# Optimization experiments

Measured on AMD Instinct MI355X. Metric: run time of the kernel, lower is better.

Reference implementation:

```python
import jax, jax.numpy as jnp
import numpy as np

N_EMB = 64
N_HEAD = 8
HEAD = N_EMB // N_HEAD
BLOCK = 64
EPS = 1e-5


def setup_inputs() -> dict:
    key = jax.random.key(0)
    ks = jax.random.split(key, 12)
    B, T, C = 4096, 64, N_EMB
    s = 0.02
    return {
        "x": jax.random.normal(ks[0], (B, T, C), jnp.float32),
        "ln1_w": jnp.ones((C,), jnp.float32),
        "ln1_b": jnp.zeros((C,), jnp.float32),
        # stacked per-head projections, layout [H, C_in, head_size] (x @ W)
        "wq": jax.random.normal(ks[1], (N_HEAD, C, HEAD), jnp.float32) * s,
        "wk": jax.random.normal(ks[2], (N_HEAD, C, HEAD), jnp.float32) * s,
        "wv": jax.random.normal(ks[3], (N_HEAD, C, HEAD), jnp.float32) * s,
        "proj_w": jax.random.normal(ks[4], (C, C), jnp.float32) * s,
        "proj_b": jnp.zeros((C,), jnp.float32),
        "ln2_w": jnp.ones((C,), jnp.float32),
        "ln2_b": jnp.zeros((C,), jnp.float32),
        "fc1_w": jax.random.normal(ks[5], (C, 4 * C), jnp.float32) * s,
        "fc1_b": jnp.zeros((4 * C,), jnp.float32),
        "fc2_w": jax.random.normal(ks[6], (4 * C, C), jnp.float32) * s,
        "fc2_b": jnp.zeros((C,), jnp.float32),
    }


def _layernorm(x, w, b):
    mu = jnp.mean(x, axis=-1, keepdims=True)
    var = jnp.mean((x - mu) ** 2, axis=-1, keepdims=True)
    return (x - mu) * jax.lax.rsqrt(var + EPS) * w + b


def reference(x, ln1_w, ln1_b, wq, wk, wv, proj_w, proj_b,
              ln2_w, ln2_b, fc1_w, fc1_b, fc2_w, fc2_b):
    B, T, C = x.shape
    # --- self-attention branch (dropout in eval mode => identity) ---
    h = _layernorm(x, ln1_w, ln1_b)
    q = jnp.einsum("btc,hcd->bhtd", h, wq)
    k = jnp.einsum("btc,hcd->bhtd", h, wk)
    v = jnp.einsum("btc,hcd->bhtd", h, wv)
    # NOTE: original scales by C**-0.5 (full embed dim), not head_size**-0.5
    scores = jnp.einsum("bhtd,bhsd->bhts", q, k) * (C ** -0.5)
    causal = jnp.tril(jnp.ones((T, T), bool))
    scores = jnp.where(causal, scores, -jnp.inf)
    w = jax.nn.softmax(scores, axis=-1)
    attn = jnp.einsum("bhts,bhsd->bhtd", w, v)  # [B,H,T,hs]
    attn = attn.transpose(0, 2, 1, 3).reshape(B, T, C)  # concat heads
    x = x + attn @ proj_w + proj_b
    # --- feed-forward branch ---
    h2 = _layernorm(x, ln2_w, ln2_b)
    ff = jax.nn.relu(h2 @ fc1_w + fc1_b) @ fc2_w + fc2_b
    return x + ff
```

## Files before the change

kernel.cpp:

```cpp
#include <hip/hip_runtime.h>

typedef __attribute__((ext_vector_type(8))) short bf16x8;
typedef __attribute__((ext_vector_type(4))) float f32x4;
typedef __attribute__((ext_vector_type(2))) unsigned int u32x2;
typedef __attribute__((ext_vector_type(4))) unsigned int u32x4;

__device__ __forceinline__ unsigned short f2bf(float f) {
  return __builtin_bit_cast(unsigned short, (__bf16)f);
}
__device__ __forceinline__ unsigned pk2(float a, float b) {
  return (unsigned)f2bf(a) | ((unsigned)f2bf(b) << 16);
}
__device__ __forceinline__ float bf2f(unsigned short h) {
  unsigned u = ((unsigned)h) << 16;
  return __builtin_bit_cast(float, u);
}
__device__ __forceinline__ bf16x8 frag(u32x4 v) { return __builtin_bit_cast(bf16x8, v); }

#if __has_builtin(__builtin_amdgcn_exp2f)
#define EXP2(x) __builtin_amdgcn_exp2f(x)
#else
#define EXP2(x) exp2f(x)
#endif

__device__ __forceinline__ void wfence() {
  asm volatile("" ::: "memory");
  __builtin_amdgcn_wave_barrier();
}

#define MFMA16(a, b, c) __builtin_amdgcn_mfma_f32_16x16x32_bf16(a, b, c, 0, 0, 0)

#define LR 72
#define OFF_VT 4608
#define OFF_Q  9216
#define ZROW   13824
#define OFF_WST 13904
#define LDS_TOT (13904 + 12288)

#define WS_H2 65536
#define WS_X2 (65536 + 16777216)

__global__ void prep_weights(const float* __restrict__ wq, const float* __restrict__ wk,
                             const float* __restrict__ wv, const float* __restrict__ projw,
                             const float* __restrict__ fc1w, const float* __restrict__ fc2w,
                             unsigned short* __restrict__ ws) {
  int c = blockIdx.x, l = threadIdx.x;
  int g = l >> 4, jl = l & 15;
  int kind, T, ks;
  if (c < 8)       { kind = 0; T = c >> 1;        ks = c & 1; }
  else if (c < 16) { kind = 1; T = (c - 8) >> 1;  ks = (c - 8) & 1; }
  else if (c < 24) { kind = 2; T = (c - 16) >> 1; ks = (c - 16) & 1; }
  else if (c < 32) { kind = 3; T = (c - 24) >> 1; ks = (c - 24) & 1; }
  else if (c < 64) { kind = 4; T = (c - 32) >> 1; ks = (c - 32) & 1; }
  else             { kind = 5; T = (c - 64) >> 3; ks = (c - 64) & 7; }
  int n = 16 * T + jl;
  unsigned short* dst = ws + c * 512 + l * 8;
  #pragma unroll
  for (int jj = 0; jj < 8; ++jj) {
    int kp = 16 * (2 * (ks & 1) + (jj >> 2)) + 4 * g + (jj & 3);
    int kn = 32 * ks + 8 * g + jj;
    float v;
    if (kind == 0)      v = wq[(n >> 3) * 512 + kp * 8 + (n & 7)] * 0.18033688011f;
    else if (kind == 1) v = wk[(n >> 3) * 512 + kp * 8 + (n & 7)];
    else if (kind == 2) v = wv[(n >> 3) * 512 + kp * 8 + (n & 7)];
    else if (kind == 3) v = projw[kn * 64 + n];
    else if (kind == 4) v = fc1w[kp * 256 + n];
    else                v = fc2w[(64 * (ks >> 1) + kp) * 64 + n];
    dst[jj] = f2bf(v);
  }
}

__global__ __launch_bounds__(256, 3) void block_attn(
    const float* __restrict__ x,
    const float* __restrict__ ln1w, const float* __restrict__ ln1b,
    const float* __restrict__ projb,
    const float* __restrict__ ln2w, const float* __restrict__ ln2b,
    unsigned short* __restrict__ wsm) {
  __shared__ __attribute__((aligned(16))) unsigned short lds[LDS_TOT];

  const int tid  = threadIdx.x;
  const int w    = tid >> 6;
  const int lane = tid & 63;
  const int g    = lane >> 4;
  const int jl   = lane & 15;
  const size_t b = blockIdx.x;
  const float* xb = x + b * 4096;
  const f32x4 zf = {0.f, 0.f, 0.f, 0.f};

  const int myrow = 16 * w + jl;
  const int krow  = myrow * LR;
  const int qrow  = OFF_Q + myrow * LR;
  const int sigb  = 32 * (w >> 1) + 8 * g + 4 * (w & 1);

  const u32x4* wsrc = (const u32x4*)wsm;
  u32x4 stg0 = wsrc[0 * 256 + tid], stg1 = wsrc[1 * 256 + tid];
  u32x4 stg2 = wsrc[2 * 256 + tid], stg3 = wsrc[3 * 256 + tid];
  u32x4 stg4 = wsrc[4 * 256 + tid], stg5 = wsrc[5 * 256 + tid];

  f32x4 xw[4];
  float mean, rstd;
  unsigned hr[8];
  {
    float s = 0.f, ss = 0.f;
    #pragma unroll
    for (int mi = 0; mi < 4; ++mi) {
      xw[mi] = *(const f32x4*)(xb + myrow * 64 + 16 * mi + 4 * g);
      #pragma unroll
      for (int r = 0; r < 4; ++r) { s += xw[mi][r]; ss += xw[mi][r] * xw[mi][r]; }
    }
    s  += __shfl_xor(s, 16, 64);  s  += __shfl_xor(s, 32, 64);
    ss += __shfl_xor(ss, 16, 64); ss += __shfl_xor(ss, 32, 64);
    mean = s * 0.015625f;
    rstd = rsqrtf(ss * 0.015625f - mean * mean + 1e-5f);
    #pragma unroll
    for (int mi = 0; mi < 4; ++mi) {
      f32x4 lw = *(const f32x4*)(ln1w + 16 * mi + 4 * g);
      f32x4 lb = *(const f32x4*)(ln1b + 16 * mi + 4 * g);
      float o0 = (xw[mi][0] - mean) * rstd * lw[0] + lb[0];
      float o1 = (xw[mi][1] - mean) * rstd * lw[1] + lb[1];
      float o2 = (xw[mi][2] - mean) * rstd * lw[2] + lb[2];
      float o3 = (xw[mi][3] - mean) * rstd * lw[3] + lb[3];
      hr[2 * mi] = pk2(o0, o1); hr[2 * mi + 1] = pk2(o2, o3);
    }
  }
  bf16x8 hb0 = frag((u32x4){hr[0], hr[1], hr[2], hr[3]});
  bf16x8 hb1 = frag((u32x4){hr[4], hr[5], hr[6], hr[7]});

  {
    u32x4* wdst = (u32x4*)(lds + OFF_WST);
    wdst[0 * 256 + tid] = stg0; wdst[1 * 256 + tid] = stg1;
    wdst[2 * 256 + tid] = stg2; wdst[3 * 256 + tid] = stg3;
    wdst[4 * 256 + tid] = stg4; wdst[5 * 256 + tid] = stg5;
  }
  if (tid < 40) ((unsigned*)(lds + ZROW))[tid] = 0u;
  __syncthreads();

  #pragma clang loop unroll(disable)
  for (int mt = 0; mt < 4; ++mt) {
    const unsigned short* wq8 = lds + OFF_WST + (2 * mt) * 512 + lane * 8;
    bf16x8 aq0 = *(const bf16x8*)(wq8);
    bf16x8 aq1 = *(const bf16x8*)(wq8 + 512);
    bf16x8 ak0 = *(const bf16x8*)(wq8 + 8 * 512);
    bf16x8 ak1 = *(const bf16x8*)(wq8 + 9 * 512);
    bf16x8 bv0 = *(const bf16x8*)(wq8 + 16 * 512);
    bf16x8 bv1 = *(const bf16x8*)(wq8 + 17 * 512);
    f32x4 q = MFMA16(aq0, hb0, zf); q = MFMA16(aq1, hb1, q);
    *(u32x2*)(lds + qrow + 16 * mt + 4 * g) = (u32x2){pk2(q[0], q[1]), pk2(q[2], q[3])};
    f32x4 kk = MFMA16(ak0, hb0, zf); kk = MFMA16(ak1, hb1, kk);
    *(u32x2*)(lds + krow + 16 * mt + 4 * g) = (u32x2){pk2(kk[0], kk[1]), pk2(kk[2], kk[3])};
    f32x4 vv = MFMA16(hb0, bv0, zf); vv = MFMA16(hb1, bv1, vv);
    *(u32x2*)(lds + OFF_VT + (16 * mt + jl) * LR + sigb) =
        (u32x2){pk2(vv[0], vv[1]), pk2(vv[2], vv[3])};
  }
  __syncthreads();

  {
    const bool g0 = (g == 0), j8 = (jl < 8);
    const int ka0 = g0 ? ((0  + jl) * LR) : ZROW;
    const int ka1 = g0 ? ((16 + jl) * LR) : ZROW;
    const int ka2 = g0 ? ((32 + jl) * LR) : ZROW;
    const int ka3 = g0 ? ((48 + jl) * LR) : ZROW;
    const int qb0 = g0 ? (OFF_Q + (0  + jl) * LR) : ZROW;
    const int qb1 = g0 ? (OFF_Q + (16 + jl) * LR) : ZROW;
    const int qb2 = g0 ? (OFF_Q + (32 + jl) * LR) : ZROW;
    const int qb3 = g0 ? (OFF_Q + (48 + jl) * LR) : ZROW;
    const bool m0 = (4 * g + 0 <= jl), m1 = (4 * g + 1 <= jl);
    const bool m2 = (4 * g + 2 <= jl), m3 = (4 * g + 3 <= jl);
    #pragma clang loop unroll(disable)
    for (int hh = 0; hh < 2; ++hh) {
      const int ho = 16 * w + 8 * hh;
      const int vbase = j8 ? (OFF_VT + (ho + jl) * LR) : ZROW;
      bf16x8 bq0 = *(const bf16x8*)(lds + qb0 + ho);
      bf16x8 bq1 = *(const bf16x8*)(lds + qb1 + ho);
      bf16x8 bq2 = *(const bf16x8*)(lds + qb2 + ho);
      bf16x8 bq3 = *(const bf16x8*)(lds + qb3 + ho);
      bf16x8 k0  = *(const bf16x8*)(lds + ka0 + ho);
      bf16x8 k1  = *(const bf16x8*)(lds + ka1 + ho);
      bf16x8 k2  = *(const bf16x8*)(lds + ka2 + ho);
      bf16x8 k3  = *(const bf16x8*)(lds + ka3 + ho);
      bf16x8 aw0 = *(const bf16x8*)(lds + vbase + 8 * g);
      bf16x8 aw1 = *(const bf16x8*)(lds + vbase + 32 + 8 * g);
      wfence();
      f32x4 s00 = MFMA16(k0, bq0, zf);
      f32x4 s10 = MFMA16(k0, bq1, zf);
      f32x4 s11 = MFMA16(k1, bq1, zf);
      {
        float e0 = m0 ? EXP2(s00[0]) : 0.f, e1 = m1 ? EXP2(s00[1]) : 0.f;
        float e2 = m2 ? EXP2(s00[2]) : 0.f, e3 = m3 ? EXP2(s00[3]) : 0.f;
        float sum = (e0 + e1) + (e2 + e3);
        sum += __shfl_xor(sum, 16, 64); sum += __shfl_xor(sum, 32, 64);
        float inv = __builtin_amdgcn_rcpf(sum);
        bf16x8 bp0 = frag((u32x4){pk2(e0, e1), pk2(e2, e3), 0u, 0u});
        f32x4 pv = MFMA16(aw0, bp0, zf);
        if (g < 2)
          *(u32x2*)(lds + OFF_Q + jl * LR + ho + 4 * g) =
              (u32x2){pk2(pv[0] * inv, pv[1] * inv), pk2(pv[2] * inv, pv[3] * inv)};
      }
      {
        float a0 = EXP2(s10[0]), a1 = EXP2(s10[1]);
        float a2 = EXP2(s10[2]), a3 = EXP2(s10[3]);
        float e0 = m0 ? EXP2(s11[0]) : 0.f, e1 = m1 ? EXP2(s11[1]) : 0.f;
        float e2 = m2 ? EXP2(s11[2]) : 0.f, e3 = m3 ? EXP2(s11[3]) : 0.f;
        float sum = ((a0 + a1) + (a2 + a3)) + ((e0 + e1) + (e2 + e3));
        sum += __shfl_xor(sum, 16, 64); sum += __shfl_xor(sum, 32, 64);
        float inv = __builtin_amdgcn_rcpf(sum);
        bf16x8 bp0 = frag((u32x4){pk2(a0, a1), pk2(a2, a3), pk2(e0, e1), pk2(e2, e3)});
        f32x4 pv = MFMA16(aw0, bp0, zf);
        if (g < 2)
          *(u32x2*)(lds + OFF_Q + (16 + jl) * LR + ho + 4 * g) =
              (u32x2){pk2(pv[0] * inv, pv[1] * inv), pk2(pv[2] * inv, pv[3] * inv)};
      }
      f32x4 s20 = MFMA16(k0, bq2, zf);
      f32x4 s21 = MFMA16(k1, bq2, zf);
      f32x4 s22 = MFMA16(k2, bq2, zf);
      f32x4 s30 = MFMA16(k0, bq3, zf);
      f32x4 s31 = MFMA16(k1, bq3, zf);
      f32x4 s32 = MFMA16(k2, bq3, zf);
      f32x4 s33 = MFMA16(k3, bq3, zf);
      {
        float a0 = EXP2(s20[0]), a1 = EXP2(s20[1]);
        float a2 = EXP2(s20[2]), a3 = EXP2(s20[3]);
        float c0 = EXP2(s21[0]), c1 = EXP2(s21[1]);
        float c2 = EXP2(s21[2]), c3 = EXP2(s21[3]);
        float e0 = m0 ? EXP2(s22[0]) : 0.f, e1 = m1 ? EXP2(s22[1]) : 0.f;
        float e2 = m2 ? EXP2(s22[2]) : 0.f, e3 = m3 ? EXP2(s22[3]) : 0.f;
        float sum = ((a0 + a1) + (a2 + a3)) + ((c0 + c1) + (c2 + c3))
                  + ((e0 + e1) + (e2 + e3));
        sum += __shfl_xor(sum, 16, 64); sum += __shfl_xor(sum, 32, 64);
        float inv = __builtin_amdgcn_rcpf(sum);
        bf16x8 bp0 = frag((u32x4){pk2(a0, a1), pk2(a2, a3), pk2(c0, c1), pk2(c2, c3)});
        bf16x8 bp1 = frag((u32x4){pk2(e0, e1), pk2(e2, e3), 0u, 0u});
        f32x4 pv = MFMA16(aw0, bp0, zf); pv = MFMA16(aw1, bp1, pv);
        if (g < 2)
          *(u32x2*)(lds + OFF_Q + (32 + jl) * LR + ho + 4 * g) =
              (u32x2){pk2(pv[0] * inv, pv[1] * inv), pk2(pv[2] * inv, pv[3] * inv)};
      }
      {
        float a0 = EXP2(s30[0]), a1 = EXP2(s30[1]);
        float a2 = EXP2(s30[2]), a3 = EXP2(s30[3]);
        float c0 = EXP2(s31[0]), c1 = EXP2(s31[1]);
        float c2 = EXP2(s31[2]), c3 = EXP2(s31[3]);
        float d0 = EXP2(s32[0]), d1 = EXP2(s32[1]);
        float d2 = EXP2(s32[2]), d3 = EXP2(s32[3]);
        float e0 = m0 ? EXP2(s33[0]) : 0.f, e1 = m1 ? EXP2(s33[1]) : 0.f;
        float e2 = m2 ? EXP2(s33[2]) : 0.f, e3 = m3 ? EXP2(s33[3]) : 0.f;
        float sum = ((a0 + a1) + (a2 + a3)) + ((c0 + c1) + (c2 + c3))
                  + ((d0 + d1) + (d2 + d3)) + ((e0 + e1) + (e2 + e3));
        sum += __shfl_xor(sum, 16, 64); sum += __shfl_xor(sum, 32, 64);
        float inv = __builtin_amdgcn_rcpf(sum);
        bf16x8 bp0 = frag((u32x4){pk2(a0, a1), pk2(a2, a3), pk2(c0, c1), pk2(c2, c3)});
        bf16x8 bp1 = frag((u32x4){pk2(d0, d1), pk2(d2, d3), pk2(e0, e1), pk2(e2, e3)});
        f32x4 pv = MFMA16(aw0, bp0, zf); pv = MFMA16(aw1, bp1, pv);
        if (g < 2)
          *(u32x2*)(lds + OFF_Q + (48 + jl) * LR + ho + 4 * g) =
              (u32x2){pk2(pv[0] * inv, pv[1] * inv), pk2(pv[2] * inv, pv[3] * inv)};
      }
    }
  }
  __syncthreads();
  bf16x8 bat0 = *(const bf16x8*)(lds + qrow + 8 * g);
  bf16x8 bat1 = *(const bf16x8*)(lds + qrow + 32 + 8 * g);

  f32x4 x2[4];
  #pragma unroll
  for (int mi = 0; mi < 4; ++mi) {
    bf16x8 a0 = *(const bf16x8*)(wsm + (24 + 2 * mi) * 512 + lane * 8);
    bf16x8 a1 = *(const bf16x8*)(wsm + (25 + 2 * mi) * 512 + lane * 8);
    f32x4 acc = MFMA16(a0, bat0, zf); acc = MFMA16(a1, bat1, acc);
    f32x4 pb = *(const f32x4*)(projb + 16 * mi + 4 * g);
    x2[mi] = xw[mi] + acc + pb;
  }

  float mean2, rstd2;
  {
    float s = 0.f, ss = 0.f;
    #pragma unroll
    for (int mi = 0; mi < 4; ++mi)
      #pragma unroll
      for (int r = 0; r < 4; ++r) { s += x2[mi][r]; ss += x2[mi][r] * x2[mi][r]; }
    s  += __shfl_xor(s, 16, 64);  s  += __shfl_xor(s, 32, 64);
    ss += __shfl_xor(ss, 16, 64); ss += __shfl_xor(ss, 32, 64);
    mean2 = s * 0.015625f;
    rstd2 = rsqrtf(ss * 0.015625f - mean2 * mean2 + 1e-5f);
  }
  unsigned h2[8];
  #pragma unroll
  for (int mi = 0; mi < 4; ++mi) {
    f32x4 lw = *(const f32x4*)(ln2w + 16 * mi + 4 * g);
    f32x4 lb = *(const f32x4*)(ln2b + 16 * mi + 4 * g);
    float o0 = (x2[mi][0] - mean2) * rstd2 * lw[0] + lb[0];
    float o1 = (x2[mi][1] - mean2) * rstd2 * lw[1] + lb[1];
    float o2 = (x2[mi][2] - mean2) * rstd2 * lw[2] + lb[2];
    float o3 = (x2[mi][3] - mean2) * rstd2 * lw[3] + lb[3];
    h2[2 * mi] = pk2(o0, o1); h2[2 * mi + 1] = pk2(o2, o3);
  }
  {
    const size_t t = b * 64 + (size_t)myrow;
    unsigned short* hrow = wsm + WS_H2 + t * 64;
    *(u32x4*)(hrow + 8 * g)      = (u32x4){h2[0], h2[1], h2[2], h2[3]};
    *(u32x4*)(hrow + 32 + 8 * g) = (u32x4){h2[4], h2[5], h2[6], h2[7]};
    unsigned short* xrow = wsm + WS_X2 + t * 64;
    #pragma unroll
    for (int mi = 0; mi < 4; ++mi)
      *(u32x2*)(xrow + 16 * mi + 4 * g) =
          (u32x2){pk2(x2[mi][0], x2[mi][1]), pk2(x2[mi][2], x2[mi][3])};
  }
}

__global__ __launch_bounds__(256, 2) void ff_stream(
    const unsigned short* __restrict__ wsm,
    const float* __restrict__ fc1b, const float* __restrict__ fc2b,
    float* __restrict__ out) {
  __shared__ __attribute__((aligned(16))) unsigned short ldsw[32768];

  const int tid  = threadIdx.x;
  const int w    = tid >> 6;
  const int lane = tid & 63;
  const int g    = lane >> 4;
  const int jl   = lane & 15;
  const int myrow = 16 * w + jl;
  const f32x4 zf = {0.f, 0.f, 0.f, 0.f};

  {
    const u32x4* src = (const u32x4*)(wsm + 16384);
    u32x4* dst = (u32x4*)ldsw;
    #pragma unroll
    for (int k = 0; k < 16; ++k) dst[k * 256 + tid] = src[k * 256 + tid];
  }
  __syncthreads();

  const unsigned short* h2g = wsm + WS_H2;
  const unsigned short* x2g = wsm + WS_X2;

  #pragma clang loop unroll(disable)
  for (int p = 0; p < 4; ++p) {
    const size_t t = (size_t)blockIdx.x * 256 + p * 64 + myrow;
    const unsigned short* hrow = h2g + t * 64;
    bf16x8 hc0 = *(const bf16x8*)(hrow + 8 * g);
    bf16x8 hc1 = *(const bf16x8*)(hrow + 32 + 8 * g);
    f32x4 x2[4];
    {
      const unsigned short* xrow = x2g + t * 64;
      #pragma unroll
      for (int mi = 0; mi < 4; ++mi) {
        u32x2 v = *(const u32x2*)(xrow + 16 * mi + 4 * g);
        x2[mi][0] = bf2f((unsigned short)(v[0] & 0xFFFF));
        x2[mi][1] = bf2f((unsigned short)(v[0] >> 16));
        x2[mi][2] = bf2f((unsigned short)(v[1] & 0xFFFF));
        x2[mi][3] = bf2f((unsigned short)(v[1] >> 16));
      }
    }
    f32x4 acc2[4];
    #pragma unroll
    for (int mi = 0; mi < 4; ++mi) acc2[mi] = zf;
    #pragma clang loop unroll(disable)
    for (int c = 0; c < 4; ++c) {
      const unsigned short* w1c = ldsw + (8 * c) * 512 + lane * 8;
      const unsigned short* w2c = ldsw + (32 + 2 * c) * 512 + lane * 8;
      const float* b1c = fc1b + 64 * c + 4 * g;
      unsigned fr0, fr1, fr2, fr3, fr4, fr5, fr6, fr7;
      {
        bf16x8 a0 = *(const bf16x8*)(w1c);
        bf16x8 a1 = *(const bf16x8*)(w1c + 512);
        f32x4 acc = MFMA16(a0, hc0, zf); acc = MFMA16(a1, hc1, acc);
        f32x4 bb = *(const f32x4*)(b1c);
        fr0 = pk2(fmaxf(acc[0] + bb[0], 0.f), fmaxf(acc[1] + bb[1], 0.f));
        fr1 = pk2(fmaxf(acc[2] + bb[2], 0.f), fmaxf(acc[3] + bb[3], 0.f));
      }
      {
        bf16x8 a0 = *(const bf16x8*)(w1c + 2 * 512);
        bf16x8 a1 = *(const bf16x8*)(w1c + 3 * 512);
        f32x4 acc = MFMA16(a0, hc0, zf); acc = MFMA16(a1, hc1, acc);
        f32x4 bb = *(const f32x4*)(b1c + 16);
        fr2 = pk2(fmaxf(acc[0] + bb[0], 0.f), fmaxf(acc[1] + bb[1], 0.f));
        fr3 = pk2(fmaxf(acc[2] + bb[2], 0.f), fmaxf(acc[3] + bb[3], 0.f));
      }
      {
        bf16x8 a0 = *(const bf16x8*)(w1c + 4 * 512);
        bf16x8 a1 = *(const bf16x8*)(w1c + 5 * 512);
        f32x4 acc = MFMA16(a0, hc0, zf); acc = MFMA16(a1, hc1, acc);
        f32x4 bb = *(const f32x4*)(b1c + 32);
        fr4 = pk2(fmaxf(acc[0] + bb[0], 0.f), fmaxf(acc[1] + bb[1], 0.f));
        fr5 = pk2(fmaxf(acc[2] + bb[2], 0.f), fmaxf(acc[3] + bb[3], 0.f));
      }
      {
        bf16x8 a0 = *(const bf16x8*)(w1c + 6 * 512);
        bf16x8 a1 = *(const bf16x8*)(w1c + 7 * 512);
        f32x4 acc = MFMA16(a0, hc0, zf); acc = MFMA16(a1, hc1, acc);
        f32x4 bb = *(const f32x4*)(b1c + 48);
        fr6 = pk2(fmaxf(acc[0] + bb[0], 0.f), fmaxf(acc[1] + bb[1], 0.f));
        fr7 = pk2(fmaxf(acc[2] + bb[2], 0.f), fmaxf(acc[3] + bb[3], 0.f));
      }
      bf16x8 bf0 = frag((u32x4){fr0, fr1, fr2, fr3});
      bf16x8 bf1 = frag((u32x4){fr4, fr5, fr6, fr7});
      #pragma unroll
      for (int mi = 0; mi < 4; ++mi) {
        bf16x8 w20 = *(const bf16x8*)(w2c + (8 * mi) * 512);
        bf16x8 w21 = *(const bf16x8*)(w2c + (8 * mi + 1) * 512);
        acc2[mi] = MFMA16(w20, bf0, acc2[mi]);
        acc2[mi] = MFMA16(w21, bf1, acc2[mi]);
      }
    }
    float* ob = out + t * 64;
    #pragma unroll
    for (int mi = 0; mi < 4; ++mi) {
      f32x4 fb = *(const f32x4*)(fc2b + 16 * mi + 4 * g);
      f32x4 o = x2[mi] + acc2[mi] + fb;
      *(f32x4*)(ob + 16 * mi + 4 * g) = o;
    }
  }
}

extern "C" void kernel_launch(void* const* d_in, const int* in_sizes, int n_in,
                              void* d_out, int out_size, void* d_ws, size_t ws_size,
                              hipStream_t stream) {
  const float* x     = (const float*)d_in[0];
  const float* ln1w  = (const float*)d_in[1];
  const float* ln1b  = (const float*)d_in[2];
  const float* wq    = (const float*)d_in[3];
  const float* wk    = (const float*)d_in[4];
  const float* wvp   = (const float*)d_in[5];
  const float* projw = (const float*)d_in[6];
  const float* projb = (const float*)d_in[7];
  const float* ln2w  = (const float*)d_in[8];
  const float* ln2b  = (const float*)d_in[9];
  const float* fc1w  = (const float*)d_in[10];
  const float* fc1b  = (const float*)d_in[11];
  const float* fc2w  = (const float*)d_in[12];
  const float* fc2b  = (const float*)d_in[13];
  unsigned short* ws = (unsigned short*)d_ws;
  float* out = (float*)d_out;

  prep_weights<<<dim3(96), dim3(64), 0, stream>>>(wq, wk, wvp, projw, fc1w, fc2w, ws);

  int nblk = in_sizes[0] / 4096;
  block_attn<<<dim3(nblk), dim3(256), 0, stream>>>(
      x, ln1w, ln1b, projb, ln2w, ln2b, ws);

  int nblk2 = (nblk * 64) / 256;
  ff_stream<<<dim3(nblk2), dim3(256), 0, stream>>>(ws, fc1b, fc2b, out);
}
```

Before: 95.22 us.

## Move LayerNorm2 into FF kernel, drop h2 intermediate, double rows per FF block

The attention kernel now writes only the post-projection residual x2 (bf16) to workspace. The second LayerNorm is recomputed inside the feed-forward kernel from that residual, so the separate h2 tensor no longer has to be written and read back through global memory. The residual is also stored with wider 16-byte vector writes. The FF kernel processes 8 row-tiles per block instead of 4, halving its grid and amortising the LDS weight load, and it hoists ln2 and fc2 bias loads out of the loop. The trade-off is extra LayerNorm arithmetic in the FF kernel and fewer blocks available for occupancy.

```diff
diff --git a/kernel.cpp b/kernel.cpp
--- a/kernel.cpp
+++ b/kernel.cpp
@@ -37,8 +37,7 @@
 #define OFF_WST 13904
 #define LDS_TOT (13904 + 12288)
 
-#define WS_H2 65536
-#define WS_X2 (65536 + 16777216)
+#define WS_X2 65536
 
 __global__ void prep_weights(const float* __restrict__ wq, const float* __restrict__ wk,
                              const float* __restrict__ wv, const float* __restrict__ projw,
@@ -74,7 +73,6 @@
     const float* __restrict__ x,
     const float* __restrict__ ln1w, const float* __restrict__ ln1b,
     const float* __restrict__ projb,
-    const float* __restrict__ ln2w, const float* __restrict__ ln2b,
     unsigned short* __restrict__ wsm) {
   __shared__ __attribute__((aligned(16))) unsigned short lds[LDS_TOT];
 
@@ -261,54 +259,43 @@
   bf16x8 bat0 = *(const bf16x8*)(lds + qrow + 8 * g);
   bf16x8 bat1 = *(const bf16x8*)(lds + qrow + 32 + 8 * g);
 
-  f32x4 x2[4];
-  #pragma unroll
-  for (int mi = 0; mi < 4; ++mi) {
-    bf16x8 a0 = *(const bf16x8*)(wsm + (24 + 2 * mi) * 512 + lane * 8);
-    bf16x8 a1 = *(const bf16x8*)(wsm + (25 + 2 * mi) * 512 + lane * 8);
-    f32x4 acc = MFMA16(a0, bat0, zf); acc = MFMA16(a1, bat1, acc);
-    f32x4 pb = *(const f32x4*)(projb + 16 * mi + 4 * g);
-    x2[mi] = xw[mi] + acc + pb;
-  }
-
-  float mean2, rstd2;
   {
-    float s = 0.f, ss = 0.f;
-    #pragma unroll
-    for (int mi = 0; mi < 4; ++mi)
-      #pragma unroll
-      for (int r = 0; r < 4; ++r) { s += x2[mi][r]; ss += x2[mi][r] * x2[mi][r]; }
-    s  += __shfl_xor(s, 16, 64);  s  += __shfl_xor(s, 32, 64);
-    ss += __shfl_xor(ss, 16, 64); ss += __shfl_xor(ss, 32, 64);
-    mean2 = s * 0.015625f;
-    rstd2 = rsqrtf(ss * 0.015625f - mean2 * mean2 + 1e-5f);
-  }
-  unsigned h2[8];
-  #pragma unroll
-  for (int mi = 0; mi < 4; ++mi) {
-    f32x4 lw = *(const f32x4*)(ln2w + 16 * mi + 4 * g);
-    f32x4 lb = *(const f32x4*)(ln2b + 16 * mi + 4 * g);
-    float o0 = (x2[mi][0] - mean2) * rstd2 * lw[0] + lb[0];
-    float o1 = (x2[mi][1] - mean2) * rstd2 * lw[1] + lb[1];
-    float o2 = (x2[mi][2] - mean2) * rstd2 * lw[2] + lb[2];
-    float o3 = (x2[mi][3] - mean2) * rstd2 * lw[3] + lb[3];
-    h2[2 * mi] = pk2(o0, o1); h2[2 * mi + 1] = pk2(o2, o3);
-  }
-  {
-    const size_t t = b * 64 + (size_t)myrow;
-    unsigned short* hrow = wsm + WS_H2 + t * 64;
-    *(u32x4*)(hrow + 8 * g)      = (u32x4){h2[0], h2[1], h2[2], h2[3]};
-    *(u32x4*)(hrow + 32 + 8 * g) = (u32x4){h2[4], h2[5], h2[6], h2[7]};
-    unsigned short* xrow = wsm + WS_X2 + t * 64;
-    #pragma unroll
-    for (int mi = 0; mi < 4; ++mi)
-      *(u32x2*)(xrow + 16 * mi + 4 * g) =
-          (u32x2){pk2(x2[mi][0], x2[mi][1]), pk2(x2[mi][2], x2[mi][3])};
+    unsigned short* xrow = wsm + WS_X2 + (b * 64 + (size_t)myrow) * 64;
+    f32x4 x20, x21, x22, x23;
+    {
+      bf16x8 a0 = *(const bf16x8*)(wsm + 24 * 512 + lane * 8);
+      bf16x8 a1 = *(const bf16x8*)(wsm + 25 * 512 + lane * 8);
+      f32x4 acc = MFMA16(a0, bat0, zf); acc = MFMA16(a1, bat1, acc);
+      x20 = xw[0] + acc + *(const f32x4*)(projb + 4 * g);
+    }
+    {
+      bf16x8 a0 = *(const bf16x8*)(wsm + 26 * 512 + lane * 8);
+      bf16x8 a1 = *(const bf16x8*)(wsm + 27 * 512 + lane * 8);
+      f32x4 acc = MFMA16(a0, bat0, zf); acc = MFMA16(a1, bat1, acc);
+      x21 = xw[1] + acc + *(const f32x4*)(projb + 16 + 4 * g);
+    }
+    *(u32x4*)(xrow + 8 * g) = (u32x4){pk2(x20[0], x20[1]), pk2(x20[2], x20[3]),
+                                      pk2(x21[0], x21[1]), pk2(x21[2], x21[3])};
+    {
+      bf16x8 a0 = *(const bf16x8*)(wsm + 28 * 512 + lane * 8);
+      bf16x8 a1 = *(const bf16x8*)(wsm + 29 * 512 + lane * 8);
+      f32x4 acc = MFMA16(a0, bat0, zf); acc = MFMA16(a1, bat1, acc);
+      x22 = xw[2] + acc + *(const f32x4*)(projb + 32 + 4 * g);
+    }
+    {
+      bf16x8 a0 = *(const bf16x8*)(wsm + 30 * 512 + lane * 8);
+      bf16x8 a1 = *(const bf16x8*)(wsm + 31 * 512 + lane * 8);
+      f32x4 acc = MFMA16(a0, bat0, zf); acc = MFMA16(a1, bat1, acc);
+      x23 = xw[3] + acc + *(const f32x4*)(projb + 48 + 4 * g);
+    }
+    *(u32x4*)(xrow + 32 + 8 * g) = (u32x4){pk2(x22[0], x22[1]), pk2(x22[2], x22[3]),
+                                           pk2(x23[0], x23[1]), pk2(x23[2], x23[3])};
   }
 }
 
 __global__ __launch_bounds__(256, 2) void ff_stream(
     const unsigned short* __restrict__ wsm,
+    const float* __restrict__ ln2w, const float* __restrict__ ln2b,
     const float* __restrict__ fc1b, const float* __restrict__ fc2b,
     float* __restrict__ out) {
   __shared__ __attribute__((aligned(16))) unsigned short ldsw[32768];
@@ -329,27 +316,55 @@
   }
   __syncthreads();
 
-  const unsigned short* h2g = wsm + WS_H2;
+  f32x4 lw2[4], lb2[4], fb2[4];
+  #pragma unroll
+  for (int mi = 0; mi < 4; ++mi) {
+    lw2[mi] = *(const f32x4*)(ln2w + 16 * mi + 4 * g);
+    lb2[mi] = *(const f32x4*)(ln2b + 16 * mi + 4 * g);
+    fb2[mi] = *(const f32x4*)(fc2b + 16 * mi + 4 * g);
+  }
+
   const unsigned short* x2g = wsm + WS_X2;
 
   #pragma clang loop unroll(disable)
-  for (int p = 0; p < 4; ++p) {
-    const size_t t = (size_t)blockIdx.x * 256 + p * 64 + myrow;
-    const unsigned short* hrow = h2g + t * 64;
-    bf16x8 hc0 = *(const bf16x8*)(hrow + 8 * g);
-    bf16x8 hc1 = *(const bf16x8*)(hrow + 32 + 8 * g);
+  for (int p = 0; p < 8; ++p) {
+    const size_t t = (size_t)blockIdx.x * 512 + p * 64 + myrow;
+    const unsigned short* xrow = x2g + t * 64;
+    u32x4 v0 = *(const u32x4*)(xrow + 8 * g);
+    u32x4 v1 = *(const u32x4*)(xrow + 32 + 8 * g);
     f32x4 x2[4];
-    {
-      const unsigned short* xrow = x2g + t * 64;
+    #pragma unroll
+    for (int q = 0; q < 2; ++q) {
+      x2[2 * q + 0][0] = bf2f((unsigned short)((q ? v1[0] : v0[0]) & 0xFFFF));
+      x2[2 * q + 0][1] = bf2f((unsigned short)((q ? v1[0] : v0[0]) >> 16));
+      x2[2 * q + 0][2] = bf2f((unsigned short)((q ? v1[1] : v0[1]) & 0xFFFF));
+      x2[2 * q + 0][3] = bf2f((unsigned short)((q ? v1[1] : v0[1]) >> 16));
+      x2[2 * q + 1][0] = bf2f((unsigned short)((q ? v1[2] : v0[2]) & 0xFFFF));
+      x2[2 * q + 1][1] = bf2f((unsigned short)((q ? v1[2] : v0[2]) >> 16));
+      x2[2 * q + 1][2] = bf2f((unsigned short)((q ? v1[3] : v0[3]) & 0xFFFF));
+      x2[2 * q + 1][3] = bf2f((unsigned short)((q ? v1[3] : v0[3]) >> 16));
+    }
+    float s = 0.f, ss = 0.f;
+    #pragma unroll
+    for (int mi = 0; mi < 4; ++mi)
       #pragma unroll
-      for (int mi = 0; mi < 4; ++mi) {
-        u32x2 v = *(const u32x2*)(xrow + 16 * mi + 4 * g);
-        x2[mi][0] = bf2f((unsigned short)(v[0] & 0xFFFF));
-        x2[mi][1] = bf2f((unsigned short)(v[0] >> 16));
-        x2[mi][2] = bf2f((unsigned short)(v[1] & 0xFFFF));
-        x2[mi][3] = bf2f((unsigned short)(v[1] >> 16));
-      }
-    }
+      for (int r = 0; r < 4; ++r) { s += x2[mi][r]; ss += x2[mi][r] * x2[mi][r]; }
+    s  += __shfl_xor(s, 16, 64);  s  += __shfl_xor(s, 32, 64);
+    ss += __shfl_xor(ss, 16, 64); ss += __shfl_xor(ss, 32, 64);
+    float mean2 = s * 0.015625f;
+    float rstd2 = rsqrtf(ss * 0.015625f - mean2 * mean2 + 1e-5f);
+    unsigned h2[8];
+    #pragma unroll
+    for (int mi = 0; mi < 4; ++mi) {
+      float o0 = (x2[mi][0] - mean2) * rstd2 * lw2[mi][0] + lb2[mi][0];
+      float o1 = (x2[mi][1] - mean2) * rstd2 * lw2[mi][1] + lb2[mi][1];
+      float o2 = (x2[mi][2] - mean2) * rstd2 * lw2[mi][2] + lb2[mi][2];
+      float o3 = (x2[mi][3] - mean2) * rstd2 * lw2[mi][3] + lb2[mi][3];
+      h2[2 * mi] = pk2(o0, o1); h2[2 * mi + 1] = pk2(o2, o3);
+    }
+    bf16x8 hc0 = frag((u32x4){h2[0], h2[1], h2[2], h2[3]});
+    bf16x8 hc1 = frag((u32x4){h2[4], h2[5], h2[6], h2[7]});
+
     f32x4 acc2[4];
     #pragma unroll
     for (int mi = 0; mi < 4; ++mi) acc2[mi] = zf;
@@ -404,8 +419,7 @@
     float* ob = out + t * 64;
     #pragma unroll
     for (int mi = 0; mi < 4; ++mi) {
-      f32x4 fb = *(const f32x4*)(fc2b + 16 * mi + 4 * g);
-      f32x4 o = x2[mi] + acc2[mi] + fb;
+      f32x4 o = x2[mi] + acc2[mi] + fb2[mi];
       *(f32x4*)(ob + 16 * mi + 4 * g) = o;
     }
   }
@@ -435,8 +449,8 @@
 
   int nblk = in_sizes[0] / 4096;
   block_attn<<<dim3(nblk), dim3(256), 0, stream>>>(
-      x, ln1w, ln1b, projb, ln2w, ln2b, ws);
-
-  int nblk2 = (nblk * 64) / 256;
-  ff_stream<<<dim3(nblk2), dim3(256), 0, stream>>>(ws, fc1b, fc2b, out);
-}
+      x, ln1w, ln1b, projb, ws);
+
+  int nblk2 = (nblk * 64) / 512;
+  ff_stream<<<dim3(nblk2), dim3(256), 0, stream>>>(ws, ln2w, ln2b, fc1b, fc2b, out);
+}
```

Result: faster. 83.24 us (-12.6%).
